# Kernel optimization log

Measured on AMD Instinct MI355X. Metric: run time of the kernel, lower is better.

The kernel has to match this reference:

```python
import jax, jax.numpy as jnp
from jax import lax
import numpy as np

WIN = 9
PAD = WIN // 2  # 4 -> SAME output size
SIM_FACTOR = 1.0
REG_FACTOR = 0.1
EPS = 1e-5

_DN = ('NCHW', 'OIHW', 'NCHW')


def box_sum(x):
    """9x9 sliding-window sum via two separable 1D ones-convs (same math as a 9x9 ones conv2d)."""
    kh = jnp.ones((1, 1, WIN, 1), x.dtype)
    kw = jnp.ones((1, 1, 1, WIN), x.dtype)
    y = lax.conv_general_dilated(x, kh, (1, 1), [(PAD, PAD), (0, 0)], dimension_numbers=_DN)
    return lax.conv_general_dilated(y, kw, (1, 1), [(0, 0), (PAD, PAD)], dimension_numbers=_DN)


def ncc2d(Ii, Ji):
    win_size = float(WIN * WIN)
    I_sum = box_sum(Ii)
    J_sum = box_sum(Ji)
    I2_sum = box_sum(Ii * Ii)
    J2_sum = box_sum(Ji * Ji)
    IJ_sum = box_sum(Ii * Ji)
    u_I = I_sum / win_size
    u_J = J_sum / win_size
    cross = IJ_sum - u_J * I_sum - u_I * J_sum + u_I * u_J * win_size
    I_var = I2_sum - 2.0 * u_I * I_sum + u_I * u_I * win_size
    J_var = J2_sum - 2.0 * u_J * J_sum + u_J * u_J * win_size
    cc = cross * cross / (I_var * J_var + EPS)
    return -jnp.mean(cc)


def grad2d_l2(y_pred):
    dy = y_pred[:, :, 1:, :] - y_pred[:, :, :-1, :]
    dx = y_pred[:, :, :, 1:] - y_pred[:, :, :, :-1]
    return (jnp.mean(dx * dx) + jnp.mean(dy * dy)) / 2.0


def setup_inputs() -> dict:
    key = jax.random.key(0)
    k1, k2, k3 = jax.random.split(key, 3)
    B, H, W = 64, 512, 512
    return {
        'target_proj': jax.random.uniform(k1, (B, 1, H, W), dtype=jnp.float32),
        'warped_moving': jax.random.uniform(k2, (B, 1, H, W), dtype=jnp.float32),
        'phi': jax.random.normal(k3, (B, 2, H, W), dtype=jnp.float32),
    }


def reference(target_proj, warped_moving, phi):
    loss_sim = ncc2d(target_proj, warped_moving) * SIM_FACTOR
    loss_reg = grad2d_l2(phi) * REG_FACTOR
    total = loss_sim + loss_reg
    return (loss_sim, loss_reg, total)
```

## Files before the change

kernel.cpp:

```cpp
#include <hip/hip_runtime.h>

#define HH 512
#define WW 512
#define RSTRIP 64
#define DRING 16

#define WAITVM(n) asm volatile("s_waitcnt vmcnt(" #n ")" ::: "memory")

__device__ __forceinline__ void gload16(const float* g, float* l) {
    __builtin_amdgcn_global_load_lds(
        (const __attribute__((address_space(1))) void*)g,
        (__attribute__((address_space(3))) void*)l, 16, 0, 0);
}

__device__ __forceinline__ void lds12(const float* __restrict__ rowp, int t,
                                      float v[12]) {
    const float4* p = reinterpret_cast<const float4*>(rowp) + t;
    float4 a = (t > 0)   ? p[-1] : make_float4(0.f, 0.f, 0.f, 0.f);
    float4 b = p[0];
    float4 c = (t < 127) ? p[1]  : make_float4(0.f, 0.f, 0.f, 0.f);
    v[0] = a.x; v[1] = a.y; v[2]  = a.z; v[3]  = a.w;
    v[4] = b.x; v[5] = b.y; v[6]  = b.z; v[7]  = b.w;
    v[8] = c.x; v[9] = c.y; v[10] = c.z; v[11] = c.w;
}

__device__ __forceinline__ void win_acc(const float d[12], float* bx) {
    float s = ((d[0] + d[1]) + (d[2] + d[3])) +
              ((d[4] + d[5]) + (d[6] + d[7])) + d[8];
    bx[0] += s;
    s += d[9]  - d[0]; bx[1] += s;
    s += d[10] - d[1]; bx[2] += s;
    s += d[11] - d[2]; bx[3] += s;
}

__device__ __forceinline__ void acc_lead(const float li[12], const float lj[12],
                                         float B[5][4]) {
    float d[12];
    win_acc(li, B[0]);
    win_acc(lj, B[1]);
#pragma unroll
    for (int c = 0; c < 12; ++c) d[c] = li[c] * li[c];
    win_acc(d, B[2]);
#pragma unroll
    for (int c = 0; c < 12; ++c) d[c] = lj[c] * lj[c];
    win_acc(d, B[3]);
#pragma unroll
    for (int c = 0; c < 12; ++c) d[c] = li[c] * lj[c];
    win_acc(d, B[4]);
}

template<bool HASL, bool HAST>
__device__ __forceinline__ void upd_lds(const float* __restrict__ Il,
                                        const float* __restrict__ Jl,
                                        const float* __restrict__ It,
                                        const float* __restrict__ Jt,
                                        int t, float B[5][4]) {
    float li[12], lj[12], ti[12], tj[12], d[12];
    if (HASL) { lds12(Il, t, li); lds12(Jl, t, lj); }
    if (HAST) { lds12(It, t, ti); lds12(Jt, t, tj); }

#pragma unroll
    for (int c = 0; c < 12; ++c)
        d[c] = HASL ? (HAST ? li[c] - ti[c] : li[c]) : -ti[c];
    win_acc(d, B[0]);
#pragma unroll
    for (int c = 0; c < 12; ++c)
        d[c] = HASL ? (HAST ? lj[c] - tj[c] : lj[c]) : -tj[c];
    win_acc(d, B[1]);
#pragma unroll
    for (int c = 0; c < 12; ++c)
        d[c] = HASL ? (HAST ? fmaf(li[c], li[c], -(ti[c] * ti[c]))
                            : li[c] * li[c])
                    : -(ti[c] * ti[c]);
    win_acc(d, B[2]);
#pragma unroll
    for (int c = 0; c < 12; ++c)
        d[c] = HASL ? (HAST ? fmaf(lj[c], lj[c], -(tj[c] * tj[c]))
                            : lj[c] * lj[c])
                    : -(tj[c] * tj[c]);
    win_acc(d, B[3]);
#pragma unroll
    for (int c = 0; c < 12; ++c)
        d[c] = HASL ? (HAST ? fmaf(li[c], lj[c], -(ti[c] * tj[c]))
                            : li[c] * lj[c])
                    : -(ti[c] * tj[c]);
    win_acc(d, B[4]);
}

__device__ __forceinline__ float cc_row(const float B[5][4]) {
    const float inv81 = 1.f / 81.f;
    float a = 0.f;
#pragma unroll
    for (int o = 0; o < 4; ++o) {
        float IS = B[0][o], JS = B[1][o];
        float I2 = B[2][o], J2 = B[3][o], IJ = B[4][o];
        float cross = fmaf(-(IS * JS), inv81, IJ);
        float Iv = fmaf(-(IS * IS), inv81, I2);
        float Jv = fmaf(-(JS * JS), inv81, J2);
        float denom = fmaf(Iv, Jv, 1e-5f);
        a = fmaf(cross * cross, __builtin_amdgcn_rcpf(denom), a);
    }
    return a;
}

__global__ __launch_bounds__(128) void ncc_kernel(const float* __restrict__ I,
                                                  const float* __restrict__ J,
                                                  float* __restrict__ ws) {
    __shared__ float ring[2][DRING][WW];
    const int T  = threadIdx.x;
    const int wv = T >> 6;
    const int b  = blockIdx.x >> 3;
    const int r0 = (blockIdx.x & 7) << 6;

    const float* Ib = I + (size_t)b * (HH * WW);
    const float* Jb = J + (size_t)b * (HH * WW);
    const int gcol = T << 2;

    if (r0 == 0) {
        const float4 z = make_float4(0.f, 0.f, 0.f, 0.f);
#pragma unroll
        for (int rr = -4; rr < 0; ++rr) {
            reinterpret_cast<float4*>(&ring[0][rr & (DRING - 1)][0])[T] = z;
            reinterpret_cast<float4*>(&ring[1][rr & (DRING - 1)][0])[T] = z;
        }
    }
    for (int rr = r0 - 4; rr <= r0 + 8; ++rr) {
        if (rr >= 0) {
            const int sl = rr & (DRING - 1);
            gload16(Ib + (size_t)rr * WW + gcol, &ring[0][sl][wv << 8]);
            gload16(Jb + (size_t)rr * WW + gcol, &ring[1][sl][wv << 8]);
        }
    }
    asm volatile("s_waitcnt vmcnt(0)" ::: "memory");
    __syncthreads();

    float B[5][4];
#pragma unroll
    for (int k = 0; k < 5; ++k)
#pragma unroll
        for (int o = 0; o < 4; ++o) B[k][o] = 0.f;

    {
        float vi[12], vj[12];
        for (int j = r0 - 4; j <= r0 + 4; ++j) {
            lds12(&ring[0][j & (DRING - 1)][0], T, vi);
            lds12(&ring[1][j & (DRING - 1)][0], T, vj);
            acc_lead(vi, vj, B);
        }
    }

    float acc = 0.f;
    for (int h = 0; h < RSTRIP; ++h) {
        WAITVM(6);
        __builtin_amdgcn_s_barrier();
        {
            const int rr = r0 + h + 9;
            const int rc = rr > HH - 1 ? HH - 1 : rr;
            const int sl = rr & (DRING - 1);
            gload16(Ib + (size_t)rc * WW + gcol, &ring[0][sl][wv << 8]);
            gload16(Jb + (size_t)rc * WW + gcol, &ring[1][sl][wv << 8]);
        }
        acc += cc_row(B);
        if (h < RSTRIP - 1) {
            const int jl = r0 + h + 5;
            const int jt = r0 + h - 4;
            const float* Ilp = &ring[0][jl & (DRING - 1)][0];
            const float* Jlp = &ring[1][jl & (DRING - 1)][0];
            const float* Itp = &ring[0][jt & (DRING - 1)][0];
            const float* Jtp = &ring[1][jt & (DRING - 1)][0];
            if (jl < HH) upd_lds<true, true>(Ilp, Jlp, Itp, Jtp, T, B);
            else         upd_lds<false, true>(Ilp, Jlp, Itp, Jtp, T, B);
        }
    }

#pragma unroll
    for (int off = 32; off; off >>= 1) acc += __shfl_down(acc, off);
    __syncthreads();
    if ((T & 63) == 0) ring[0][0][wv] = acc;
    __syncthreads();
    if (T == 0) atomicAdd(&ws[0], ring[0][0][0] + ring[0][0][1]);
}

__global__ __launch_bounds__(256) void reg_kernel(const float* __restrict__ P,
                                                  float* __restrict__ ws) {
    __shared__ float sh[8];
    const int T = threadIdx.x;
    const int c4 = T & 127;
    const int strip = (blockIdx.x << 1) | (T >> 7);
    const size_t row0 = (size_t)strip << 5;
    const bool slast = ((strip & 15) == 15);
    const float* rp = P + row0 * WW + (c4 << 2);

    float sdx = 0.f, sdy = 0.f;
    float4 cur = *reinterpret_cast<const float4*>(rp);
#pragma unroll 8
    for (int i = 0; i < 32; ++i) {
        float d0 = cur.y - cur.x, d1 = cur.z - cur.y, d2 = cur.w - cur.z;
        sdx += d0 * d0 + d1 * d1 + d2 * d2;
        if (c4 < 127) {
            float nx = rp[(size_t)i * WW + 4];
            float d3 = nx - cur.w;
            sdx += d3 * d3;
        }
        if (i < 31) {
            float4 nr = *reinterpret_cast<const float4*>(rp + (size_t)(i + 1) * WW);
            float e0 = nr.x - cur.x, e1 = nr.y - cur.y;
            float e2 = nr.z - cur.z, e3 = nr.w - cur.w;
            sdy += e0 * e0 + e1 * e1 + e2 * e2 + e3 * e3;
            cur = nr;
        } else if (!slast) {
            float4 nr = *reinterpret_cast<const float4*>(rp + (size_t)32 * WW);
            float e0 = nr.x - cur.x, e1 = nr.y - cur.y;
            float e2 = nr.z - cur.z, e3 = nr.w - cur.w;
            sdy += e0 * e0 + e1 * e1 + e2 * e2 + e3 * e3;
        }
    }

#pragma unroll
    for (int off = 32; off; off >>= 1) {
        sdx += __shfl_down(sdx, off);
        sdy += __shfl_down(sdy, off);
    }
    if ((T & 63) == 0) { sh[T >> 6] = sdx; sh[4 + (T >> 6)] = sdy; }
    __syncthreads();
    if (T == 0) {
        atomicAdd(&ws[1], sh[0] + sh[1] + sh[2] + sh[3]);
        atomicAdd(&ws[2], sh[4] + sh[5] + sh[6] + sh[7]);
    }
}

__global__ void finalize_kernel(const float* __restrict__ ws,
                                float* __restrict__ out) {
    float cc_sum = ws[0], dx_sum = ws[1], dy_sum = ws[2];
    float loss_sim = -(cc_sum / 16777216.f);
    float mdx = dx_sum / 33488896.f;
    float mdy = dy_sum / 33488896.f;
    float loss_reg = (mdx + mdy) * 0.5f * 0.1f;
    out[0] = loss_sim;
    out[1] = loss_reg;
    out[2] = loss_sim + loss_reg;
}

extern "C" void kernel_launch(void* const* d_in, const int* in_sizes, int n_in,
                              void* d_out, int out_size, void* d_ws, size_t ws_size,
                              hipStream_t stream) {
    const float* I = (const float*)d_in[0];
    const float* J = (const float*)d_in[1];
    const float* P = (const float*)d_in[2];
    float* out = (float*)d_out;
    float* ws = (float*)d_ws;

    hipMemsetAsync(d_ws, 0, 3 * sizeof(float), stream);
    ncc_kernel<<<512, 128, 0, stream>>>(I, J, ws);
    reg_kernel<<<1024, 256, 0, stream>>>(P, ws);
    finalize_kernel<<<1, 1, 0, stream>>>(ws, out);
}
```

Before: 119.2 us.

## Double threads per NCC block with padded LDS rows and register double-buffering

The NCC kernel now runs 256 threads per block, each computing 2 output columns instead of 4. Each LDS row is padded with zero halos, so the window reads become unconditional float2 loads. Window reads for the next row are prefetched into alternating register sets, and the load ring runs two rows further ahead. The regularisation kernel uses 16-row strips and twice as many blocks. The aim is more parallelism and latency hiding, at the cost of more LDS reads per output and higher register pressure.

```diff
diff --git a/kernel.cpp b/kernel.cpp
--- a/kernel.cpp
+++ b/kernel.cpp
@@ -3,7 +3,8 @@
 #define HH 512
 #define WW 512
 #define RSTRIP 64
-#define DRING 16
+#define DR 16
+#define PW 520
 
 #define WAITVM(n) asm volatile("s_waitcnt vmcnt(" #n ")" ::: "memory")
 
@@ -13,85 +14,88 @@
         (__attribute__((address_space(3))) void*)l, 16, 0, 0);
 }
 
-__device__ __forceinline__ void lds12(const float* __restrict__ rowp, int t,
-                                      float v[12]) {
-    const float4* p = reinterpret_cast<const float4*>(rowp) + t;
-    float4 a = (t > 0)   ? p[-1] : make_float4(0.f, 0.f, 0.f, 0.f);
-    float4 b = p[0];
-    float4 c = (t < 127) ? p[1]  : make_float4(0.f, 0.f, 0.f, 0.f);
-    v[0] = a.x; v[1] = a.y; v[2]  = a.z; v[3]  = a.w;
-    v[4] = b.x; v[5] = b.y; v[6]  = b.z; v[7]  = b.w;
-    v[8] = c.x; v[9] = c.y; v[10] = c.z; v[11] = c.w;
-}
-
-__device__ __forceinline__ void win_acc(const float d[12], float* bx) {
-    float s = ((d[0] + d[1]) + (d[2] + d[3])) +
-              ((d[4] + d[5]) + (d[6] + d[7])) + d[8];
-    bx[0] += s;
-    s += d[9]  - d[0]; bx[1] += s;
-    s += d[10] - d[1]; bx[2] += s;
-    s += d[11] - d[2]; bx[3] += s;
-}
-
-__device__ __forceinline__ void acc_lead(const float li[12], const float lj[12],
-                                         float B[5][4]) {
-    float d[12];
-    win_acc(li, B[0]);
-    win_acc(lj, B[1]);
-#pragma unroll
-    for (int c = 0; c < 12; ++c) d[c] = li[c] * li[c];
-    win_acc(d, B[2]);
-#pragma unroll
-    for (int c = 0; c < 12; ++c) d[c] = lj[c] * lj[c];
-    win_acc(d, B[3]);
-#pragma unroll
-    for (int c = 0; c < 12; ++c) d[c] = li[c] * lj[c];
-    win_acc(d, B[4]);
-}
-
-template<bool HASL, bool HAST>
-__device__ __forceinline__ void upd_lds(const float* __restrict__ Il,
-                                        const float* __restrict__ Jl,
-                                        const float* __restrict__ It,
-                                        const float* __restrict__ Jt,
-                                        int t, float B[5][4]) {
-    float li[12], lj[12], ti[12], tj[12], d[12];
-    if (HASL) { lds12(Il, t, li); lds12(Jl, t, lj); }
-    if (HAST) { lds12(It, t, ti); lds12(Jt, t, tj); }
-
-#pragma unroll
-    for (int c = 0; c < 12; ++c)
-        d[c] = HASL ? (HAST ? li[c] - ti[c] : li[c]) : -ti[c];
-    win_acc(d, B[0]);
-#pragma unroll
-    for (int c = 0; c < 12; ++c)
-        d[c] = HASL ? (HAST ? lj[c] - tj[c] : lj[c]) : -tj[c];
-    win_acc(d, B[1]);
-#pragma unroll
-    for (int c = 0; c < 12; ++c)
-        d[c] = HASL ? (HAST ? fmaf(li[c], li[c], -(ti[c] * ti[c]))
-                            : li[c] * li[c])
-                    : -(ti[c] * ti[c]);
-    win_acc(d, B[2]);
-#pragma unroll
-    for (int c = 0; c < 12; ++c)
-        d[c] = HASL ? (HAST ? fmaf(lj[c], lj[c], -(tj[c] * tj[c]))
-                            : lj[c] * lj[c])
-                    : -(tj[c] * tj[c]);
-    win_acc(d, B[3]);
-#pragma unroll
-    for (int c = 0; c < 12; ++c)
-        d[c] = HASL ? (HAST ? fmaf(li[c], lj[c], -(ti[c] * tj[c]))
-                            : li[c] * lj[c])
-                    : -(ti[c] * tj[c]);
-    win_acc(d, B[4]);
-}
-
-__device__ __forceinline__ float cc_row(const float B[5][4]) {
+__device__ __forceinline__ void rdwin(const float* __restrict__ rowp, int t,
+                                      float (&w)[10]) {
+    const float2* p = reinterpret_cast<const float2*>(rowp) + t;
+#pragma unroll
+    for (int i = 0; i < 5; ++i) {
+        float2 x = p[i];
+        w[2 * i] = x.x;
+        w[2 * i + 1] = x.y;
+    }
+}
+
+__device__ __forceinline__ void fold2(const float d[10], float* b) {
+    float s = (((d[0] + d[1]) + (d[2] + d[3])) +
+               ((d[4] + d[5]) + (d[6] + d[7]))) + d[8];
+    b[0] += s;
+    s += d[9] - d[0];
+    b[1] += s;
+}
+
+__device__ __forceinline__ void acc_lead2(const float (&wi)[10],
+                                          const float (&wj)[10],
+                                          float (&B)[5][2]) {
+    float d[10];
+    fold2(wi, B[0]);
+    fold2(wj, B[1]);
+#pragma unroll
+    for (int i = 0; i < 10; ++i) d[i] = wi[i] * wi[i];
+    fold2(d, B[2]);
+#pragma unroll
+    for (int i = 0; i < 10; ++i) d[i] = wj[i] * wj[i];
+    fold2(d, B[3]);
+#pragma unroll
+    for (int i = 0; i < 10; ++i) d[i] = wi[i] * wj[i];
+    fold2(d, B[4]);
+}
+
+__device__ __forceinline__ void upd2_full(const float (&li)[10], const float (&lj)[10],
+                                          const float (&ti)[10], const float (&tj)[10],
+                                          float (&B)[5][2]) {
+    float d[10];
+#pragma unroll
+    for (int i = 0; i < 10; ++i) d[i] = li[i] - ti[i];
+    fold2(d, B[0]);
+#pragma unroll
+    for (int i = 0; i < 10; ++i) d[i] = lj[i] - tj[i];
+    fold2(d, B[1]);
+#pragma unroll
+    for (int i = 0; i < 10; ++i) d[i] = fmaf(li[i], li[i], -(ti[i] * ti[i]));
+    fold2(d, B[2]);
+#pragma unroll
+    for (int i = 0; i < 10; ++i) d[i] = fmaf(lj[i], lj[i], -(tj[i] * tj[i]));
+    fold2(d, B[3]);
+#pragma unroll
+    for (int i = 0; i < 10; ++i) d[i] = fmaf(li[i], lj[i], -(ti[i] * tj[i]));
+    fold2(d, B[4]);
+}
+
+__device__ __forceinline__ void upd2_trail(const float (&ti)[10], const float (&tj)[10],
+                                           float (&B)[5][2]) {
+    float d[10];
+#pragma unroll
+    for (int i = 0; i < 10; ++i) d[i] = -ti[i];
+    fold2(d, B[0]);
+#pragma unroll
+    for (int i = 0; i < 10; ++i) d[i] = -tj[i];
+    fold2(d, B[1]);
+#pragma unroll
+    for (int i = 0; i < 10; ++i) d[i] = -(ti[i] * ti[i]);
+    fold2(d, B[2]);
+#pragma unroll
+    for (int i = 0; i < 10; ++i) d[i] = -(tj[i] * tj[i]);
+    fold2(d, B[3]);
+#pragma unroll
+    for (int i = 0; i < 10; ++i) d[i] = -(ti[i] * tj[i]);
+    fold2(d, B[4]);
+}
+
+__device__ __forceinline__ float cc2(const float (&B)[5][2]) {
     const float inv81 = 1.f / 81.f;
     float a = 0.f;
 #pragma unroll
-    for (int o = 0; o < 4; ++o) {
+    for (int o = 0; o < 2; ++o) {
         float IS = B[0][o], JS = B[1][o];
         float I2 = B[2][o], J2 = B[3][o], IJ = B[4][o];
         float cross = fmaf(-(IS * JS), inv81, IJ);
@@ -103,82 +107,105 @@
     return a;
 }
 
-__global__ __launch_bounds__(128) void ncc_kernel(const float* __restrict__ I,
+__global__ __launch_bounds__(256) void ncc_kernel(const float* __restrict__ I,
                                                   const float* __restrict__ J,
                                                   float* __restrict__ ws) {
-    __shared__ float ring[2][DRING][WW];
-    const int T  = threadIdx.x;
+    __shared__ float ring[2][DR][PW];
+    const int T = threadIdx.x;
     const int wv = T >> 6;
-    const int b  = blockIdx.x >> 3;
+    const int lane = T & 63;
+    const int b = blockIdx.x >> 3;
     const int r0 = (blockIdx.x & 7) << 6;
 
     const float* Ib = I + (size_t)b * (HH * WW);
     const float* Jb = J + (size_t)b * (HH * WW);
-    const int gcol = T << 2;
-
+    const int img = wv >> 1;
+    const int half = wv & 1;
+    const float* src_base = img ? Jb : Ib;
+
+    {
+        const int pimg = T >> 7;
+        const int psl = (T >> 3) & 15;
+        const int k = T & 7;
+        ring[pimg][psl][(k < 4) ? k : (512 + k)] = 0.f;
+    }
     if (r0 == 0) {
-        const float4 z = make_float4(0.f, 0.f, 0.f, 0.f);
-#pragma unroll
-        for (int rr = -4; rr < 0; ++rr) {
-            reinterpret_cast<float4*>(&ring[0][rr & (DRING - 1)][0])[T] = z;
-            reinterpret_cast<float4*>(&ring[1][rr & (DRING - 1)][0])[T] = z;
-        }
-    }
-    for (int rr = r0 - 4; rr <= r0 + 8; ++rr) {
+#pragma unroll
+        for (int q = 0; q < 4; ++q) {
+            const int id = q * 256 + T;
+            const int zimg = id >> 9;
+            const int rem = id & 511;
+            const int zsl = 12 + (rem >> 7);
+            reinterpret_cast<float4*>(&ring[zimg][zsl][4])[rem & 127] =
+                make_float4(0.f, 0.f, 0.f, 0.f);
+        }
+    }
+    for (int rr = r0 - 4; rr <= r0 + 10; ++rr) {
         if (rr >= 0) {
-            const int sl = rr & (DRING - 1);
-            gload16(Ib + (size_t)rr * WW + gcol, &ring[0][sl][wv << 8]);
-            gload16(Jb + (size_t)rr * WW + gcol, &ring[1][sl][wv << 8]);
+            gload16(src_base + (size_t)rr * WW + (half << 8) + (lane << 2),
+                    &ring[img][rr & 15][4 + (half << 8)]);
         }
     }
     asm volatile("s_waitcnt vmcnt(0)" ::: "memory");
     __syncthreads();
 
-    float B[5][4];
-#pragma unroll
-    for (int k = 0; k < 5; ++k)
-#pragma unroll
-        for (int o = 0; o < 4; ++o) B[k][o] = 0.f;
-
-    {
-        float vi[12], vj[12];
-        for (int j = r0 - 4; j <= r0 + 4; ++j) {
-            lds12(&ring[0][j & (DRING - 1)][0], T, vi);
-            lds12(&ring[1][j & (DRING - 1)][0], T, vj);
-            acc_lead(vi, vj, B);
-        }
-    }
+    float B[5][2];
+#pragma unroll
+    for (int k = 0; k < 5; ++k) { B[k][0] = 0.f; B[k][1] = 0.f; }
+
+    for (int j = r0 - 4; j <= r0 + 4; ++j) {
+        float wi[10], wj[10];
+        rdwin(&ring[0][j & 15][0], T, wi);
+        rdwin(&ring[1][j & 15][0], T, wj);
+        acc_lead2(wi, wj, B);
+    }
+
+    float Ali[10], Alj[10], Ati[10], Atj[10];
+    float Bli[10], Blj[10], Bti[10], Btj[10];
+    rdwin(&ring[0][(r0 + 5) & 15][0], T, Ali);
+    rdwin(&ring[1][(r0 + 5) & 15][0], T, Alj);
+    rdwin(&ring[0][(r0 - 4) & 15][0], T, Ati);
+    rdwin(&ring[1][(r0 - 4) & 15][0], T, Atj);
 
     float acc = 0.f;
-    for (int h = 0; h < RSTRIP; ++h) {
-        WAITVM(6);
-        __builtin_amdgcn_s_barrier();
-        {
-            const int rr = r0 + h + 9;
-            const int rc = rr > HH - 1 ? HH - 1 : rr;
-            const int sl = rr & (DRING - 1);
-            gload16(Ib + (size_t)rc * WW + gcol, &ring[0][sl][wv << 8]);
-            gload16(Jb + (size_t)rc * WW + gcol, &ring[1][sl][wv << 8]);
-        }
-        acc += cc_row(B);
-        if (h < RSTRIP - 1) {
-            const int jl = r0 + h + 5;
-            const int jt = r0 + h - 4;
-            const float* Ilp = &ring[0][jl & (DRING - 1)][0];
-            const float* Jlp = &ring[1][jl & (DRING - 1)][0];
-            const float* Itp = &ring[0][jt & (DRING - 1)][0];
-            const float* Jtp = &ring[1][jt & (DRING - 1)][0];
-            if (jl < HH) upd_lds<true, true>(Ilp, Jlp, Itp, Jtp, T, B);
-            else         upd_lds<false, true>(Ilp, Jlp, Itp, Jtp, T, B);
-        }
-    }
+
+#define STEP(h, CLi, CLj, CTi, CTj, NLi, NLj, NTi, NTj)                       \
+    {                                                                         \
+        WAITVM(4);                                                            \
+        __builtin_amdgcn_s_barrier();                                         \
+        {   \
+            const int rr = r0 + (h) + 11;                                     \
+            const int rc = rr > HH - 1 ? HH - 1 : rr;                         \
+            gload16(src_base + (size_t)rc * WW + (half << 8) + (lane << 2),   \
+                    &ring[img][rr & 15][4 + (half << 8)]);                    \
+        }                                                                     \
+        acc += cc2(B);                                                        \
+        if ((h) < RSTRIP - 1) {                                               \
+            if (r0 + (h) + 5 < HH) upd2_full(CLi, CLj, CTi, CTj, B);          \
+            else                   upd2_trail(CTi, CTj, B);                   \
+            const int jl = r0 + (h) + 6, jt = r0 + (h) - 3;                   \
+            rdwin(&ring[0][jl & 15][0], T, NLi);                              \
+            rdwin(&ring[1][jl & 15][0], T, NLj);                              \
+            rdwin(&ring[0][jt & 15][0], T, NTi);                              \
+            rdwin(&ring[1][jt & 15][0], T, NTj);                              \
+        }                                                                     \
+    }
+
+    for (int k = 0; k < RSTRIP / 2; ++k) {
+        const int h0 = 2 * k, h1 = 2 * k + 1;
+        STEP(h0, Ali, Alj, Ati, Atj, Bli, Blj, Bti, Btj);
+        STEP(h1, Bli, Blj, Bti, Btj, Ali, Alj, Ati, Atj);
+    }
+#undef STEP
 
 #pragma unroll
     for (int off = 32; off; off >>= 1) acc += __shfl_down(acc, off);
     __syncthreads();
-    if ((T & 63) == 0) ring[0][0][wv] = acc;
-    __syncthreads();
-    if (T == 0) atomicAdd(&ws[0], ring[0][0][0] + ring[0][0][1]);
+    if (lane == 0) ring[0][0][wv] = acc;
+    __syncthreads();
+    if (T == 0)
+        atomicAdd(&ws[0], (ring[0][0][0] + ring[0][0][1]) +
+                          (ring[0][0][2] + ring[0][0][3]));
 }
 
 __global__ __launch_bounds__(256) void reg_kernel(const float* __restrict__ P,
@@ -187,14 +214,14 @@
     const int T = threadIdx.x;
     const int c4 = T & 127;
     const int strip = (blockIdx.x << 1) | (T >> 7);
-    const size_t row0 = (size_t)strip << 5;
-    const bool slast = ((strip & 15) == 15);
+    const size_t row0 = (size_t)strip << 4;
+    const bool slast = ((strip & 31) == 31);
     const float* rp = P + row0 * WW + (c4 << 2);
 
     float sdx = 0.f, sdy = 0.f;
     float4 cur = *reinterpret_cast<const float4*>(rp);
 #pragma unroll 8
-    for (int i = 0; i < 32; ++i) {
+    for (int i = 0; i < 16; ++i) {
         float d0 = cur.y - cur.x, d1 = cur.z - cur.y, d2 = cur.w - cur.z;
         sdx += d0 * d0 + d1 * d1 + d2 * d2;
         if (c4 < 127) {
@@ -202,14 +229,14 @@
             float d3 = nx - cur.w;
             sdx += d3 * d3;
         }
-        if (i < 31) {
+        if (i < 15) {
             float4 nr = *reinterpret_cast<const float4*>(rp + (size_t)(i + 1) * WW);
             float e0 = nr.x - cur.x, e1 = nr.y - cur.y;
             float e2 = nr.z - cur.z, e3 = nr.w - cur.w;
             sdy += e0 * e0 + e1 * e1 + e2 * e2 + e3 * e3;
             cur = nr;
         } else if (!slast) {
-            float4 nr = *reinterpret_cast<const float4*>(rp + (size_t)32 * WW);
+            float4 nr = *reinterpret_cast<const float4*>(rp + (size_t)16 * WW);
             float e0 = nr.x - cur.x, e1 = nr.y - cur.y;
             float e2 = nr.z - cur.z, e3 = nr.w - cur.w;
             sdy += e0 * e0 + e1 * e1 + e2 * e2 + e3 * e3;
@@ -251,7 +278,7 @@
     float* ws = (float*)d_ws;
 
     hipMemsetAsync(d_ws, 0, 3 * sizeof(float), stream);
-    ncc_kernel<<<512, 128, 0, stream>>>(I, J, ws);
-    reg_kernel<<<1024, 256, 0, stream>>>(P, ws);
+    ncc_kernel<<<512, 256, 0, stream>>>(I, J, ws);
+    reg_kernel<<<2048, 256, 0, stream>>>(P, ws);
     finalize_kernel<<<1, 1, 0, stream>>>(ws, out);
 }
```

New measurement: 137.8 us. 1.16x slower.
